# Optimization experiments

Measured on AMD Instinct MI355X. Metric: run time of the kernel, lower is better.

Reference implementation:

```python
import jax, jax.numpy as jnp
import numpy as np
from jax import lax

B, C, HH, WW, M, DS = 16, 80, 128, 128, 32, 4
H_IMG, W_IMG = HH * DS, WW * DS


def setup_inputs() -> dict:
    key = jax.random.key(0)
    k = jax.random.split(key, 8)
    # head outputs: hm is sigmoid-activated in (0,1); sz/os are ReLU outputs (>=0)
    hm = jax.nn.sigmoid(jax.random.normal(k[0], (B, C, HH, WW), jnp.float32))
    sz = jax.random.uniform(k[1], (B, 2, HH, WW), jnp.float32) * 64.0
    os_ = jax.random.uniform(k[2], (B, 2, HH, WW), jnp.float32)
    # ground-truth boxes (xmin,ymin,xmax,ymax) inside the 512x512 image
    x1 = jax.random.uniform(k[3], (B, M), jnp.float32) * 440.0
    y1 = jax.random.uniform(k[4], (B, M), jnp.float32) * 440.0
    w = jax.random.uniform(k[5], (B, M), jnp.float32) * 60.0 + 8.0
    h = jax.random.uniform(k[6], (B, M), jnp.float32) * 60.0 + 8.0
    gt_bboxes = jnp.stack([x1, y1, x1 + w, y1 + h], -1)
    gt_classes = jax.random.randint(k[7], (B, M), 0, C, jnp.int32)
    return {"hm": hm, "sz": sz, "os": os_, "gt_bboxes": gt_bboxes, "gt_classes": gt_classes}


def _smooth_l1(p, g):
    d = jnp.abs(p - g)
    return jnp.where(d < 1.0, 0.5 * d * d, d - 0.5)


def reference(hm, sz, os, gt_bboxes, gt_classes):
    dt = hm.dtype
    # ---- NMS via 3x3 max-pool, keep only local maxima ----
    hmax = lax.reduce_window(hm, -jnp.inf, lax.max, (1, 1, 3, 3), (1, 1, 1, 1), "SAME")
    peaks = jnp.where(hm == hmax, hm, jnp.zeros((), dt)).transpose(0, 2, 3, 1)  # [B,H,W,C]
    values = peaks.max(-1)      # [B,H,W] best score per pixel
    idxs = peaks.argmax(-1)     # [B,H,W] class index
    keep = values > 0
    # ---- dense bbox decode (same math as the nonzero/gather loop, mask instead) ----
    szp = sz.transpose(0, 2, 3, 1)  # [B,H,W,2]
    osp = os.transpose(0, 2, 3, 1)
    pts = jnp.stack(jnp.meshgrid(jnp.arange(HH), jnp.arange(WW), indexing="ij"), -1).astype(dt)
    ctr = pts * DS + osp
    bb = jnp.concatenate([ctr - szp / 2, ctr + szp / 2], -1)  # [B,H,W,4]
    bboxes = jnp.stack([
        jnp.clip(bb[..., 0], 0.0, W_IMG), jnp.clip(bb[..., 1], 0.0, H_IMG),
        jnp.clip(bb[..., 2], 0.0, W_IMG), jnp.clip(bb[..., 3], 0.0, H_IMG)], -1)
    # ---- build gt heatmap / size / offset targets (vectorized gaussian splat) ----
    cxy = (gt_bboxes[..., :2] + gt_bboxes[..., 2:]) / 2          # [B,M,2]
    cpts = jnp.floor(cxy / DS)                                    # [B,M,2]
    sizes = gt_bboxes[..., 2:] - gt_bboxes[..., :2]               # [B,M,2]
    offs = cxy / DS - cpts                                        # [B,M,2]
    ci = cpts.astype(jnp.int32)
    bidx = jnp.broadcast_to(jnp.arange(B)[:, None], (B, M))
    gt_sz = jnp.zeros((B, HH, WW, 2), dt).at[bidx, ci[..., 0], ci[..., 1]].set(sizes)
    gt_os = jnp.zeros((B, HH, WW, 2), dt).at[bidx, ci[..., 0], ci[..., 1]].set(offs)
    sigma = sizes.max(-1) / DS                                    # [B,M] (note: not squared, as in source)
    d2 = ((pts[None, None] - cpts[:, :, None, None, :]) ** 2).sum(-1)   # [B,M,H,W]
    gauss = jnp.exp(-d2 / (2.0 * sigma[:, :, None, None]))
    seg = (bidx * C + gt_classes).reshape(-1)
    gt_hm = jax.ops.segment_max(gauss.reshape(B * M, HH, WW), seg, num_segments=B * C)
    gt_hm = jnp.maximum(gt_hm.reshape(B, C, HH, WW), 0.0)
    # ---- losses ----
    keep_tr = (gt_hm == 1.0).sum(1) > 0            # [B,H,W] center pixels
    n = keep_tr.sum().astype(dt)
    mask = keep_tr[..., None].astype(dt)
    size_loss = (_smooth_l1(szp, gt_sz) * mask).sum() / (2.0 * n) / n
    offset_loss = (_smooth_l1(osp, gt_os) * mask).sum() / (2.0 * n) / n
    fl = (1 - gt_hm) ** 4 * hm ** 2 * jnp.log1p(-hm) + gt_hm ** 4 * (1 - hm) ** 2 * jnp.log(hm)
    point_focal_loss = -fl.sum()
    return (values, idxs, bboxes, keep, point_focal_loss, size_loss, offset_loss, gt_hm)
```

## Files before the change

kernel.cpp:

```cpp
#include <hip/hip_runtime.h>
#include <math.h>

#define NB 16
#define NC 80
#define HH 128
#define WW 128
#define HW (HH*WW)
#define HW4 (HW/4)
#define NPIX (NB*HH*WW)
#define NM 32
#define IMG 512.0f
#define NW 8
#define NCL (NC/NW)
#define MAIN_BLOCKS (NB*64)

#define OFF_VALUES 0
#define OFF_IDXS   262144
#define OFF_BBOX   524288
#define OFF_KEEP   1572864
#define OFF_PFL    1835008
#define OFF_SZL    1835009
#define OFF_OSL    1835010
#define OFF_GTHM   1835011

#define WS_BPS   0
#define WS_CSRS  8192
#define WS_FPART 13376

typedef float vfloat4 __attribute__((ext_vector_type(4)));

__device__ __forceinline__ float smooth_l1(float p, float g) {
    float d = fabsf(p - g);
    return (d < 1.0f) ? 0.5f * d * d : d - 0.5f;
}
__device__ __forceinline__ float fmax3(float a, float b, float c) {
    return fmaxf(fmaxf(a, b), c);
}

__global__ void setup_kernel(const float* __restrict__ gtb, const int* __restrict__ gtc,
                             float4* __restrict__ bps, int* __restrict__ csr_start) {
    __shared__ float4 s_bp[NB * NM];
    __shared__ int    s_cls[NB * NM];
    __shared__ int    s_pos[NB][NC];
    int t = threadIdx.x;
    {
        const float* g = gtb + t * 4;
        float x1 = g[0], y1 = g[1], x2 = g[2], y2 = g[3];
        float cx = (x1 + x2) * 0.5f, cy = (y1 + y2) * 0.5f;
        float c0 = floorf(cx * 0.25f);
        float c1 = floorf(cy * 0.25f);
        float w = x2 - x1, h = y2 - y1;
        float sigma = fmaxf(w, h) * 0.25f;
        float4 p;
        p.x = c0; p.y = c1;
        p.z = 1.0f / (2.0f * sigma);
        p.w = 0.0f;
        s_bp[t] = p;
        s_cls[t] = gtc[t];
    }
    __syncthreads();
    for (int e = t; e < NB * (NC + 1); e += 512) {
        int b = e / (NC + 1), c = e - b * (NC + 1);
        int cnt = 0;
        #pragma unroll
        for (int m = 0; m < NM; ++m) cnt += (s_cls[b * NM + m] < c) ? 1 : 0;
        csr_start[e] = cnt;
        if (c < NC) s_pos[b][c] = cnt;
    }
    __syncthreads();
    {
        int b = t >> 5;
        int c = s_cls[t];
        int slot = atomicAdd(&s_pos[b][c], 1);
        bps[b * NM + slot] = s_bp[t];
    }
}

__launch_bounds__(512, 8)
__global__ void main_kernel(const float* __restrict__ hm,
                            const float* __restrict__ sz,
                            const float* __restrict__ osr,
                            const float4* __restrict__ bps,
                            const int* __restrict__ csr_start,
                            float* __restrict__ fpart,
                            float* __restrict__ out) {
    int blk = blockIdx.x;
    int b = blk >> 6;
    int i0 = (blk & 63) << 1;
    int tid = threadIdx.x;
    int wid = tid >> 6;
    int lane = tid & 63;
    int lane31 = lane & 31;
    int r = lane >> 5;
    int i = i0 + r;
    int jb = lane31 << 2;
    int c0 = wid * NCL;

    __shared__ int    s_start[NC + 1];
    __shared__ float4 s_box[NM];
    __shared__ float  s_val[NW][256];
    __shared__ unsigned char s_cls[NW][256];
    __shared__ float  s_red[NW];

    for (int k = tid; k < NC + 1; k += 512) s_start[k] = csr_start[b * (NC + 1) + k];
    if (tid < NM) s_box[tid] = bps[b * NM + tid];
    __syncthreads();

    const float fi = (float)i, fjb = (float)jb;
    int iu  = (i > 0) ? i - 1 : 0;
    int idn = (i < HH - 1) ? i + 1 : HH - 1;
    size_t base = ((size_t)b * NC + c0) * HW;

    const float4* pC = (const float4*)(hm + base + i   * WW + jb);
    const float4* pU = (const float4*)(hm + base + iu  * WW + jb);
    const float4* pD = (const float4*)(hm + base + idn * WW + jb);
    float* gp = out + OFF_GTHM + base + i * WW + jb;

    bool clampL = (lane31 == 0);
    bool clampR = (lane31 == 31);
    int srcG = (lane & 32) | ((lane31 + 1) & 31);

    float bestv[4] = {-1.f, -1.f, -1.f, -1.f};
    int   bestc[4] = {0, 0, 0, 0};
    float facc = 0.0f;

    auto process = [&](float4 cC, float4 cU, float4 cD, int cc, float* gpc) {
        int c = c0 + cc;
        int s0 = s_start[c], s1 = s_start[c + 1];

        float h[4] = {cC.x, cC.y, cC.z, cC.w};
        float vm[4];
        vm[0] = fmax3(cU.x, h[0], cD.x);
        vm[1] = fmax3(cU.y, h[1], cD.y);
        vm[2] = fmax3(cU.z, h[2], cD.z);
        vm[3] = fmax3(cU.w, h[3], cD.w);
        float left  = __shfl_up(vm[3], 1);
        float right = __shfl_down(vm[0], 1);
        if (clampL) left  = vm[0];
        if (clampR) right = vm[3];
        float mx[4];
        mx[0] = fmax3(left,  vm[0], vm[1]);
        mx[1] = fmax3(vm[0], vm[1], vm[2]);
        mx[2] = fmax3(vm[1], vm[2], vm[3]);
        mx[3] = fmax3(vm[2], vm[3], right);
        #pragma unroll
        for (int k = 0; k < 4; ++k) {
            float p = (h[k] >= mx[k]) ? h[k] : 0.0f;
            if (p > bestv[k]) { bestv[k] = p; bestc[k] = cc; }
        }

        float gv[4] = {0.f, 0.f, 0.f, 0.f};
        for (int kk = s0; kk < s1; ++kk) {
            float4 bx = s_box[kk];
            float d0 = fi - bx.x;
            float nis = -bx.z;
            float dj = fjb - bx.y;
            float e = d0 * d0;
            #pragma unroll
            for (int k = 0; k < 4; ++k) {
                float d1 = dj + (float)k;
                gv[k] = fmaxf(gv[k], __expf((e + d1 * d1) * nis));
            }
        }

        #pragma unroll
        for (int k = 0; k < 4; ++k) {
            float hk = h[k], ohk = 1.0f - hk;
            float gk = gv[k], omk = 1.0f - gk;
            float om2 = omk * omk, g2 = gk * gk;
            facc += (om2 * om2) * hk * hk * __logf(ohk)
                  + (g2 * g2) * ohk * ohk * __logf(hk);
        }

        float g4th = __shfl(gv[0], srcG);
        if (lane31 != 31) {
            vfloat4 sv = {gv[1], gv[2], gv[3], g4th};
            *(vfloat4*)(gpc + 1) = sv;
        } else {
            gpc[1] = gv[1];
            gpc[2] = gv[2];
            gpc[3] = gv[3];
            gpc[-124] = g4th;
        }
    };

    float4 cC = *pC, cU = *pU, cD = *pD;
    for (int cc = 0; cc < NCL - 1; ++cc) {
        float4 nC = pC[HW4], nU = pU[HW4], nD = pD[HW4];
        process(cC, cU, cD, cc, gp);
        pC += HW4; pU += HW4; pD += HW4; gp += HW;
        cC = nC; cU = nU; cD = nD;
    }
    process(cC, cU, cD, NCL - 1, gp);

    int pl = r * 128 + jb;
    float4 bv4 = {bestv[0], bestv[1], bestv[2], bestv[3]};
    *(float4*)&s_val[wid][pl] = bv4;
    unsigned int cpk = (unsigned)bestc[0] | ((unsigned)bestc[1] << 8) |
                       ((unsigned)bestc[2] << 16) | ((unsigned)bestc[3] << 24);
    *(unsigned int*)&s_cls[wid][pl] = cpk;

    #pragma unroll
    for (int off = 32; off > 0; off >>= 1) facc += __shfl_down(facc, off);
    if (lane == 0) s_red[wid] = facc;
    __syncthreads();

    if (tid < 256) {
        float bv = -1.0f; int bi = 0;
        #pragma unroll
        for (int g2 = 0; g2 < NW; ++g2) {
            float v = s_val[g2][tid];
            if (v > bv) { bv = v; bi = g2 * NCL + (int)s_cls[g2][tid]; }
        }
        int rr  = tid >> 7;
        int col = tid & 127;
        int ij  = (i0 + rr) * WW + col;
        int pix = b * HW + ij;
        out[OFF_VALUES + pix] = bv;
        out[OFF_IDXS + pix]   = (float)bi;
        out[OFF_KEEP + pix]   = (bv > 0.0f) ? 1.0f : 0.0f;

        const float* szb = sz  + (size_t)b * 2 * HW;
        const float* osb = osr + (size_t)b * 2 * HW;
        float s0v = szb[ij], s1v = szb[HW + ij];
        float o0 = osb[ij],  o1 = osb[HW + ij];
        float cx = (float)(i0 + rr) * 4.0f + o0;
        float cy = (float)col * 4.0f + o1;
        float4 bb;
        bb.x = fminf(fmaxf(cx - s0v * 0.5f, 0.0f), IMG);
        bb.y = fminf(fmaxf(cy - s1v * 0.5f, 0.0f), IMG);
        bb.z = fminf(fmaxf(cx + s0v * 0.5f, 0.0f), IMG);
        bb.w = fminf(fmaxf(cy + s1v * 0.5f, 0.0f), IMG);
        reinterpret_cast<float4*>(out + OFF_BBOX)[pix] = bb;
    }
    if (tid == 0) {
        float t = 0.0f;
        #pragma unroll
        for (int g2 = 0; g2 < NW; ++g2) t += s_red[g2];
        fpart[blk] = t;
    }
}

__global__ void loss_kernel(const float* __restrict__ gtb, const float* __restrict__ sz,
                            const float* __restrict__ osr, const float* __restrict__ fpart,
                            float* __restrict__ out) {
    int t = threadIdx.x;
    int b = t >> 5, m = t & 31;
    __shared__ int s_ci[NB * NM];
    const float* g = gtb + t * 4;
    float x1 = g[0], y1 = g[1], x2 = g[2], y2 = g[3];
    float cx = (x1 + x2) * 0.5f, cy = (y1 + y2) * 0.5f;
    float c0f = floorf(cx * 0.25f), c1f = floorf(cy * 0.25f);
    int ci0 = (int)c0f, ci1 = (int)c1f;
    s_ci[t] = ci0 * WW + ci1;
    __syncthreads();

    bool winner = true;
    int mycell = s_ci[t];
    for (int m2 = m + 1; m2 < NM; ++m2)
        if (s_ci[b * NM + m2] == mycell) { winner = false; break; }

    float nloc = 0.0f, szs = 0.0f, oss = 0.0f;
    if (winner) {
        nloc = 1.0f;
        float w = x2 - x1, h = y2 - y1;
        float offx = cx * 0.25f - c0f, offy = cy * 0.25f - c1f;
        size_t pb = (size_t)b * 2 * HW + (size_t)ci0 * WW + ci1;
        float ps0 = sz[pb], ps1 = sz[pb + HW];
        float po0 = osr[pb], po1 = osr[pb + HW];
        szs = smooth_l1(ps0, w) + smooth_l1(ps1, h);
        oss = smooth_l1(po0, offx) + smooth_l1(po1, offy);
    }

    float fsum = fpart[t] + fpart[t + 512];

    #pragma unroll
    for (int off = 32; off > 0; off >>= 1) {
        nloc += __shfl_down(nloc, off);
        szs  += __shfl_down(szs, off);
        oss  += __shfl_down(oss, off);
        fsum += __shfl_down(fsum, off);
    }
    __shared__ float red[8][4];
    int wid = t >> 6;
    if ((t & 63) == 0) { red[wid][0] = nloc; red[wid][1] = szs; red[wid][2] = oss; red[wid][3] = fsum; }
    __syncthreads();
    if (t == 0) {
        float n = 0.0f, ss = 0.0f, os_ = 0.0f, ft = 0.0f;
        for (int w2 = 0; w2 < 8; ++w2) { n += red[w2][0]; ss += red[w2][1]; os_ += red[w2][2]; ft += red[w2][3]; }
        out[OFF_SZL] = ss / (2.0f * n) / n;
        out[OFF_OSL] = os_ / (2.0f * n) / n;
        out[OFF_PFL] = -ft;
    }
}

extern "C" void kernel_launch(void* const* d_in, const int* in_sizes, int n_in,
                              void* d_out, int out_size, void* d_ws, size_t ws_size,
                              hipStream_t stream) {
    const float* hm  = (const float*)d_in[0];
    const float* sz  = (const float*)d_in[1];
    const float* osr = (const float*)d_in[2];
    const float* gtb = (const float*)d_in[3];
    const int*   gtc = (const int*)d_in[4];
    float* out = (float*)d_out;

    float4* bps    = (float4*)((char*)d_ws + WS_BPS);
    int* csr_start = (int*)((char*)d_ws + WS_CSRS);
    float* fpart   = (float*)((char*)d_ws + WS_FPART);

    setup_kernel<<<1, 512, 0, stream>>>(gtb, gtc, bps, csr_start);
    main_kernel<<<MAIN_BLOCKS, 512, 0, stream>>>(hm, sz, osr, bps, csr_start, fpart, out);
    loss_kernel<<<1, 512, 0, stream>>>(gtb, sz, osr, fpart, out);
}
```

Baseline: 58.03 us.

## Share neighbor rows across half-waves and skip gaussian work for empty classes

Each wave covers two adjacent rows, so the other row's center values are now fetched with a cross-half shuffle. Each lane loads only the one outer halo row it needs, which cuts global loads per channel from three float4 to two. When a class has no boxes in the image, the focal-loss term reduces to h^2*log(1-h) and skips the gt-dependent log and multiplies. This adds four shuffles per channel and a branch, which is uniform across the wave because it depends only on the class.

Measured after the change: 55.96 us, median of 2. -3.6%, faster.

```diff
diff --git a/kernel.cpp b/kernel.cpp
--- a/kernel.cpp
+++ b/kernel.cpp
@@ -107,13 +107,11 @@
     __syncthreads();
 
     const float fi = (float)i, fjb = (float)jb;
-    int iu  = (i > 0) ? i - 1 : 0;
-    int idn = (i < HH - 1) ? i + 1 : HH - 1;
+    int hrow = r ? ((i < HH - 1) ? i + 1 : HH - 1) : ((i > 0) ? i - 1 : 0);
     size_t base = ((size_t)b * NC + c0) * HW;
 
-    const float4* pC = (const float4*)(hm + base + i   * WW + jb);
-    const float4* pU = (const float4*)(hm + base + iu  * WW + jb);
-    const float4* pD = (const float4*)(hm + base + idn * WW + jb);
+    const float4* pC = (const float4*)(hm + base + i    * WW + jb);
+    const float4* pH = (const float4*)(hm + base + hrow * WW + jb);
     float* gp = out + OFF_GTHM + base + i * WW + jb;
 
     bool clampL = (lane31 == 0);
@@ -124,16 +122,20 @@
     int   bestc[4] = {0, 0, 0, 0};
     float facc = 0.0f;
 
-    auto process = [&](float4 cC, float4 cU, float4 cD, int cc, float* gpc) {
+    auto process = [&](float4 cC, float4 cH, int cc, float* gpc) {
         int c = c0 + cc;
         int s0 = s_start[c], s1 = s_start[c + 1];
 
         float h[4] = {cC.x, cC.y, cC.z, cC.w};
+        float o0 = __shfl_xor(cC.x, 32);
+        float o1 = __shfl_xor(cC.y, 32);
+        float o2 = __shfl_xor(cC.z, 32);
+        float o3 = __shfl_xor(cC.w, 32);
         float vm[4];
-        vm[0] = fmax3(cU.x, h[0], cD.x);
-        vm[1] = fmax3(cU.y, h[1], cD.y);
-        vm[2] = fmax3(cU.z, h[2], cD.z);
-        vm[3] = fmax3(cU.w, h[3], cD.w);
+        vm[0] = fmax3(h[0], cH.x, o0);
+        vm[1] = fmax3(h[1], cH.y, o1);
+        vm[2] = fmax3(h[2], cH.z, o2);
+        vm[3] = fmax3(h[3], cH.w, o3);
         float left  = __shfl_up(vm[3], 1);
         float right = __shfl_down(vm[0], 1);
         if (clampL) left  = vm[0];
@@ -150,26 +152,33 @@
         }
 
         float gv[4] = {0.f, 0.f, 0.f, 0.f};
-        for (int kk = s0; kk < s1; ++kk) {
-            float4 bx = s_box[kk];
-            float d0 = fi - bx.x;
-            float nis = -bx.z;
-            float dj = fjb - bx.y;
-            float e = d0 * d0;
+        if (s0 != s1) {
+            for (int kk = s0; kk < s1; ++kk) {
+                float4 bx = s_box[kk];
+                float d0 = fi - bx.x;
+                float nis = -bx.z;
+                float dj = fjb - bx.y;
+                float e = d0 * d0;
+                #pragma unroll
+                for (int k = 0; k < 4; ++k) {
+                    float d1 = dj + (float)k;
+                    gv[k] = fmaxf(gv[k], __expf((e + d1 * d1) * nis));
+                }
+            }
             #pragma unroll
             for (int k = 0; k < 4; ++k) {
-                float d1 = dj + (float)k;
-                gv[k] = fmaxf(gv[k], __expf((e + d1 * d1) * nis));
+                float hk = h[k], ohk = 1.0f - hk;
+                float gk = gv[k], omk = 1.0f - gk;
+                float om2 = omk * omk, g2 = gk * gk;
+                facc += (om2 * om2) * hk * hk * __logf(ohk)
+                      + (g2 * g2) * ohk * ohk * __logf(hk);
             }
-        }
-
-        #pragma unroll
-        for (int k = 0; k < 4; ++k) {
-            float hk = h[k], ohk = 1.0f - hk;
-            float gk = gv[k], omk = 1.0f - gk;
-            float om2 = omk * omk, g2 = gk * gk;
-            facc += (om2 * om2) * hk * hk * __logf(ohk)
-                  + (g2 * g2) * ohk * ohk * __logf(hk);
+        } else {
+            #pragma unroll
+            for (int k = 0; k < 4; ++k) {
+                float hk = h[k];
+                facc += hk * hk * __logf(1.0f - hk);
+            }
         }
 
         float g4th = __shfl(gv[0], srcG);
@@ -184,14 +193,14 @@
         }
     };
 
-    float4 cC = *pC, cU = *pU, cD = *pD;
+    float4 cC = *pC, cH = *pH;
     for (int cc = 0; cc < NCL - 1; ++cc) {
-        float4 nC = pC[HW4], nU = pU[HW4], nD = pD[HW4];
-        process(cC, cU, cD, cc, gp);
-        pC += HW4; pU += HW4; pD += HW4; gp += HW;
-        cC = nC; cU = nU; cD = nD;
-    }
-    process(cC, cU, cD, NCL - 1, gp);
+        float4 nC = pC[HW4], nH = pH[HW4];
+        process(cC, cH, cc, gp);
+        pC += HW4; pH += HW4; gp += HW;
+        cC = nC; cH = nH;
+    }
+    process(cC, cH, NCL - 1, gp);
 
     int pl = r * 128 + jb;
     float4 bv4 = {bestv[0], bestv[1], bestv[2], bestv[3]};
```
